# Performance work log

Measured on AMD Instinct MI355X. Metric: run time of the kernel, lower is better.

Reference implementation:

```python
import jax, jax.numpy as jnp
import numpy as np

B, N, M = 8, 2048, 16
HA, HB, HG = 64, 32, 32
NCONV, VOCAB, HINIT = 4, 100, 92
NAMINO = 2048
EPS = 1e-5


def setup_inputs() -> dict:
    key = jax.random.key(0)
    ks = jax.random.split(key, 24)
    s = 0.02
    return {
        'atom_emb_idx': jax.random.randint(ks[0], (B, N), 0, VOCAB, dtype=jnp.int32),
        'nbr_emb': jax.random.normal(ks[1], (B, N, M, HB), jnp.float32),
        'nbr_adj_list': jax.random.randint(ks[2], (B, N, M), 0, N, dtype=jnp.int32),
        'atom_amino_idx': jax.random.randint(ks[3], (B, N), 0, NAMINO, dtype=jnp.int32),
        'atom_mask': jnp.ones((B, N), jnp.float32),
        'embed_table': jax.random.normal(ks[4], (VOCAB, HINIT), jnp.float32) * s,
        'W_emb': jax.random.normal(ks[5], (HINIT, HA), jnp.float32) * s,
        'b_emb': jnp.zeros((HA,), jnp.float32),
        'fc_W': jax.random.normal(ks[6], (NCONV, 2 * HA + HB, 2 * HA), jnp.float32) * s,
        'fc_b': jnp.zeros((NCONV, 2 * HA), jnp.float32),
        'bnh_g': jnp.ones((NCONV, 2 * HA), jnp.float32),
        'bnh_b': jnp.zeros((NCONV, 2 * HA), jnp.float32),
        'bno_g': jnp.ones((NCONV, HA), jnp.float32),
        'bno_b': jnp.zeros((NCONV, HA), jnp.float32),
        'W_cf': jax.random.normal(ks[7], (HA, HG), jnp.float32) * s,
        'b_cf': jnp.zeros((HG,), jnp.float32),
        'W_out': jax.random.normal(ks[8], (HG, 1), jnp.float32) * s,
        'b_out': jnp.zeros((1,), jnp.float32),
        'W_af': jax.random.normal(ks[9], (HA, HG), jnp.float32) * s,
        'b_af': jnp.zeros((HG,), jnp.float32),
        'W_ao': jax.random.normal(ks[10], (HG, 1), jnp.float32) * s,
        'b_ao': jnp.zeros((1,), jnp.float32),
    }


def _bn(x, g, b, axes):
    # training-mode batchnorm (biased variance), matching torch default train()
    m = jnp.mean(x, axis=axes, keepdims=True)
    v = jnp.mean((x - m) ** 2, axis=axes, keepdims=True)
    return (x - m) * jax.lax.rsqrt(v + EPS) * g + b


def _conv(atom_emb, nbr_emb, adj, mask, W, b, g1, be1, g2, be2):
    # atom_emb [B,N,HA], adj [B,N,M], mask [B,N,1]
    nbr_atom = jax.vmap(lambda e, i: e[i])(atom_emb, adj)       # gather [B,N,M,HA]
    nbr_atom = nbr_atom * mask[..., None]                        # [B,N,1,1] bcast
    self_emb = jnp.broadcast_to(atom_emb[:, :, None, :], nbr_atom.shape)
    tot = jnp.concatenate([self_emb, nbr_atom, nbr_emb], axis=-1)  # [B,N,M,2HA+HB]
    z = tot @ W + b                                              # [B,N,M,2HA]
    z = _bn(z, g1, be1, (0, 1, 2))
    filt, core = jnp.split(z, 2, axis=-1)
    s = jnp.sum(jax.nn.sigmoid(filt) * jax.nn.relu(core), axis=2)  # [B,N,HA]
    s = _bn(s, g2, be2, (0, 1))
    return jax.nn.relu(atom_emb + s)


def reference(atom_emb_idx, nbr_emb, nbr_adj_list, atom_amino_idx, atom_mask,
              embed_table, W_emb, b_emb, fc_W, fc_b, bnh_g, bnh_b, bno_g, bno_b,
              W_cf, b_cf, W_out, b_out, W_af, b_af, W_ao, b_ao):
    atom_emb = embed_table[atom_emb_idx] @ W_emb + b_emb        # [B,N,HA]
    mask = atom_mask[..., None]                                  # [B,N,1]
    for i in range(NCONV):
        atom_emb = atom_emb * mask
        atom_emb = _conv(atom_emb, nbr_emb, nbr_adj_list, mask,
                         fc_W[i], fc_b[i], bnh_g[i], bnh_b[i], bno_g[i], bno_b[i])
    atom_emb = atom_emb * mask
    # residue (amino) pooling via scatter-add
    idx = atom_amino_idx.reshape(-1)
    amino_emb = jax.ops.segment_sum(atom_emb.reshape(-1, HA), idx, num_segments=NAMINO)
    mask_pooled = jnp.where(jnp.arange(NAMINO)[:, None] < jnp.min(idx), 0, 1).astype(jnp.uint8)
    amino_emb = jax.nn.relu(amino_emb) @ W_af + b_af
    amino_emb = jax.nn.relu(amino_emb)
    # protein pooling: masked mean
    protein_emb = jnp.sum(atom_emb, axis=1) / jnp.sum(mask, axis=1)  # [B,HA]
    protein_emb = jax.nn.relu(protein_emb) @ W_cf + b_cf
    protein_emb = jax.nn.relu(protein_emb)
    out_global = protein_emb @ W_out + b_out                     # [B,1]
    out_amino = amino_emb @ W_ao + b_ao                          # [NAMINO,1]
    return out_global, out_amino, mask_pooled
```

## Files before the change

### kernel.cpp

```cpp
#include <hip/hip_runtime.h>
#include <cstdint>
#include <cstddef>

#define EPS_ 1e-5f
#define NATOM 16384
#define NB    8
#define NN    2048
#define NM    16
#define NHA   64
#define NHB   32
#define NHG   32
#define NVOCAB 100
#define NHINIT 92
#define NAMINO_ 2048
#define NPART 1024
#define NSLOT 8

#define OFF_EMB      0
#define OFF_SELF     1048576
#define OFF_NBRU     3145728
#define OFF_S        4194304
#define OFF_AMINO    5242880
#define OFF_PSUM     5373952
#define OFF_MSUM     5374464
#define OFF_MAX      5374472
#define OFF_SLOT1    5374480
#define OFF_SLOT2    5382672
#define ZERO_FLOATS  (5386768 - 5242880)
#define OFF_PACK     5386768
#define OFF_WPACK    9581072
#define WS_FLOATS    9589264

typedef __attribute__((ext_vector_type(8))) short bf16x8;
typedef __attribute__((ext_vector_type(4))) float f32x4;

static __device__ __forceinline__ short f2bf(float f) {
    union { float f; uint32_t u; } v; v.f = f;
    uint32_t r = v.u + 0x7fffu + ((v.u >> 16) & 1u);
    return (short)(r >> 16);
}
static __device__ __forceinline__ float bfLo(uint32_t x) {
    union { uint32_t u; float f; } v; v.u = x << 16; return v.f;
}
static __device__ __forceinline__ float bfHi(uint32_t x) {
    union { uint32_t u; float f; } v; v.u = x & 0xffff0000u; return v.f;
}

static __device__ __forceinline__ int conv_wg(int bid) {
    return (bid & 7) * (NPART / 8) + (bid >> 3);
}

__launch_bounds__(256)
__global__ void k_prep(const float* __restrict__ nbr_emb, uint4* __restrict__ pack,
                       const int* __restrict__ atom_idx, const float* __restrict__ et,
                       const float* __restrict__ W_emb, const float* __restrict__ b_emb,
                       float* __restrict__ emb,
                       const float* __restrict__ fcW, uint4* __restrict__ wpack)
{
    __shared__ float lw[NHINIT * NHA];
    const int t = threadIdx.x;
    if (blockIdx.x < 4096) {
        int g = blockIdx.x * 256 + t;
        int bn = g >> 6, l = g & 63;
        const float* src = nbr_emb + (size_t)bn * 512 + (l & 15) * 32 + (l >> 4) * 8;
        float4 a = *reinterpret_cast<const float4*>(src);
        float4 b = *reinterpret_cast<const float4*>(src + 4);
        union { short s[8]; uint4 u; } o;
        o.s[0] = f2bf(a.x); o.s[1] = f2bf(a.y); o.s[2] = f2bf(a.z); o.s[3] = f2bf(a.w);
        o.s[4] = f2bf(b.x); o.s[5] = f2bf(b.y); o.s[6] = f2bf(b.z); o.s[7] = f2bf(b.w);
        pack[g] = o.u;
        return;
    }
    if (blockIdx.x >= 5120) {
        int L = blockIdx.x - 5120;
        if (t < 64) {
            int l15 = t & 15, lg = t >> 4;
            const float* We = fcW + (size_t)L * 160 * 128 + 128 * 128;
#pragma unroll
            for (int cb = 0; cb < 8; ++cb) {
                union { short s[8]; uint4 u; } w;
#pragma unroll
                for (int j = 0; j < 8; ++j)
                    w.s[j] = f2bf(We[(lg * 8 + j) * 128 + cb * 16 + l15]);
                wpack[L * 512 + cb * 64 + t] = w.u;
            }
        }
        return;
    }
    for (int j = t; j < NHINIT * NHA; j += 256) lw[j] = W_emb[j];
    __syncthreads();
    const int bbase = (blockIdx.x - 4096) * 16;
    const int sub = t >> 6, c = t & 63;
    const float bb = b_emb[c];
#pragma unroll
    for (int aa = 0; aa < 4; ++aa) {
        int atom = bbase + sub + 4 * aa;
        int idxu = __builtin_amdgcn_readfirstlane(atom_idx[atom]);
        const float* er = et + (size_t)idxu * NHINIT;
        float acc = bb;
        for (int h = 0; h < NHINIT; ++h)
            acc = fmaf(er[h], lw[h * NHA + c], acc);
        emb[(size_t)atom * NHA + c] = acc;
    }
}

template<int UPD>
__launch_bounds__(256)
__global__ void k_proj(float* __restrict__ emb, const float* __restrict__ mask,
                       const float* __restrict__ s_buf, const float* __restrict__ slot2,
                       const float* __restrict__ g1, const float* __restrict__ b1,
                       const float* __restrict__ fcW, const float* __restrict__ fcb,
                       float* __restrict__ selfp, uint32_t* __restrict__ nbrpU)
{
    __shared__ float le[512];
    __shared__ float nb[8][128];
    __shared__ float affA[64], affB[64];
    const int t = threadIdx.x;
    if (UPD) {
        if (t < 64) {
            float S = 0.f, Q = 0.f;
#pragma unroll
            for (int s = 0; s < NSLOT; ++s) {
                S += slot2[s * 128 + t];
                Q += slot2[s * 128 + 64 + t];
            }
            float mean = S * (1.f / 16384.f);
            float var = Q * (1.f / 16384.f) - mean * mean;
            float a = g1[t] * rsqrtf(var + EPS_);
            affA[t] = a; affB[t] = b1[t] - mean * a;
        }
        __syncthreads();
    }
#pragma unroll
    for (int jj = 0; jj < 2; ++jj) {
        int j = t + jj * 256;
        int gi = blockIdx.x * 512 + j;
        int bn = blockIdx.x * 8 + (j >> 6);
        int c = j & 63;
        float m = mask[bn];
        float v;
        if (UPD) {
            v = fmaxf(fmaf(s_buf[gi], affA[c], affB[c]) + emb[gi] * m, 0.f);
            emb[gi] = v;
        } else {
            v = emb[gi];
        }
        le[j] = v * m;
    }
    __syncthreads();
    int half = t >> 7;
    int oc = t & 127;
    float acc[8];
    float bias = half ? 0.f : fcb[oc];
#pragma unroll
    for (int a = 0; a < 8; ++a) acc[a] = bias;
    const float* Wbase = fcW + (half * 64) * 128 + oc;
    for (int c = 0; c < 64; ++c) {
        float w = Wbase[c * 128];
#pragma unroll
        for (int a = 0; a < 8; ++a) acc[a] = fmaf(le[a * 64 + c], w, acc[a]);
    }
    if (half == 0) {
#pragma unroll
        for (int a = 0; a < 8; ++a)
            selfp[(size_t)(blockIdx.x * 8 + a) * 128 + oc] = acc[a];
    } else {
#pragma unroll
        for (int a = 0; a < 8; ++a) nb[a][oc] = acc[a];
    }
    __syncthreads();
#pragma unroll
    for (int k = 0; k < 2; ++k) {
        int idx = t + k * 256;
        int a = idx >> 6, c2 = idx & 63;
        uint32_t lo = (uint16_t)f2bf(nb[a][c2]);
        uint32_t hi = (uint16_t)f2bf(nb[a][c2 + 64]);
        nbrpU[(size_t)(blockIdx.x * 8 + a) * 64 + c2] = lo | (hi << 16);
    }
}

__launch_bounds__(256, 4)
__global__ void k_conv_stats(const float* __restrict__ selfp, const uint32_t* __restrict__ nbrpU,
                             const uint4* __restrict__ pack, const int* __restrict__ adj,
                             const float* __restrict__ mask, const uint4* __restrict__ wpack,
                             float* __restrict__ slot1)
{
    __shared__ float red[4][256];
    const int lane = threadIdx.x & 63;
    const int wid = threadIdx.x >> 6;
    const int l15 = lane & 15, lg = lane >> 4;
    bf16x8 Wb[8];
#pragma unroll
    for (int cb = 0; cb < 8; ++cb) {
        union { uint4 u; bf16x8 v; } w;
        w.u = wpack[cb * 64 + lane];
        Wb[cb] = w.v;
    }
    float sum[8] = {0, 0, 0, 0, 0, 0, 0, 0};
    float sq[8] = {0, 0, 0, 0, 0, 0, 0, 0};
    const int wg = conv_wg(blockIdx.x);
    const int base = (wg * 4 + wid) * 4;
    for (int aa = 0; aa < 4; ++aa) {
        const int bn = base + aa;
        const int b = bn >> 11;
        const float mn = mask[bn];
        int adjv = 0;
        if (lane < 16) adjv = adj[bn * 16 + lane];
        union { uint4 u; bf16x8 v; } af;
        af.u = pack[(size_t)bn * 64 + lane];
        float sp[8];
#pragma unroll
        for (int cb = 0; cb < 8; ++cb) sp[cb] = selfp[(size_t)bn * 128 + cb * 16 + l15];
        const uint32_t* npb = nbrpU + (size_t)b * NN * 64;
        f32x4 acc[8];
#pragma unroll
        for (int r = 0; r < 4; ++r) {
            const int am = __shfl(adjv, lg * 4 + r);
            const uint32_t* rowU = npb + (size_t)am * 64;
#pragma unroll
            for (int c2 = 0; c2 < 4; ++c2) {
                uint32_t u = rowU[c2 * 16 + l15];
                acc[c2][r]     = fmaf(mn, bfLo(u), sp[c2]);
                acc[c2 + 4][r] = fmaf(mn, bfHi(u), sp[c2 + 4]);
            }
        }
#pragma unroll
        for (int cb = 0; cb < 8; ++cb)
            acc[cb] = __builtin_amdgcn_mfma_f32_16x16x32_bf16(af.v, Wb[cb], acc[cb], 0, 0, 0);
#pragma unroll
        for (int cb = 0; cb < 8; ++cb) {
#pragma unroll
            for (int r = 0; r < 4; ++r) {
                float z = acc[cb][r];
                sum[cb] += z; sq[cb] = fmaf(z, z, sq[cb]);
            }
        }
    }
#pragma unroll
    for (int cb = 0; cb < 8; ++cb) {
        sum[cb] += __shfl_xor(sum[cb], 16);
        sum[cb] += __shfl_xor(sum[cb], 32);
        sq[cb] += __shfl_xor(sq[cb], 16);
        sq[cb] += __shfl_xor(sq[cb], 32);
    }
    if (lane < 16) {
#pragma unroll
        for (int cb = 0; cb < 8; ++cb) {
            red[wid][cb * 16 + lane] = sum[cb];
            red[wid][128 + cb * 16 + lane] = sq[cb];
        }
    }
    __syncthreads();
    const int t = threadIdx.x;
    float v = red[0][t] + red[1][t] + red[2][t] + red[3][t];
    atomicAdd(&slot1[(blockIdx.x & (NSLOT - 1)) * 256 + t], v);
}

__launch_bounds__(256, 4)
__global__ void k_conv_gate(const float* __restrict__ selfp, const uint32_t* __restrict__ nbrpU,
                            const uint4* __restrict__ pack, const int* __restrict__ adj,
                            const float* __restrict__ mask, const uint4* __restrict__ wpack,
                            const float* __restrict__ slot1,
                            const float* __restrict__ g0, const float* __restrict__ b0,
                            float* __restrict__ s_out, float* __restrict__ slot2)
{
    __shared__ float red[4][128];
    __shared__ float a1[128], b1s[128];
    const int t = threadIdx.x;
    if (t < 128) {
        float S = 0.f, Q = 0.f;
#pragma unroll
        for (int s = 0; s < NSLOT; ++s) {
            S += slot1[s * 256 + t];
            Q += slot1[s * 256 + 128 + t];
        }
        float mean = S * (1.f / 262144.f);
        float var = Q * (1.f / 262144.f) - mean * mean;
        float a = g0[t] * rsqrtf(var + EPS_);
        a1[t] = a; b1s[t] = b0[t] - mean * a;
    }
    __syncthreads();
    const int lane = threadIdx.x & 63;
    const int wid = threadIdx.x >> 6;
    const int l15 = lane & 15, lg = lane >> 4;
    bf16x8 Wb[8];
#pragma unroll
    for (int cb = 0; cb < 8; ++cb) {
        union { uint4 u; bf16x8 v; } w;
        w.u = wpack[cb * 64 + lane];
        Wb[cb] = w.v;
    }
    float aA[8], aB[8];
#pragma unroll
    for (int cb = 0; cb < 8; ++cb) {
        aA[cb] = a1[cb * 16 + l15];
        aB[cb] = b1s[cb * 16 + l15];
    }
    float ssum[4] = {0, 0, 0, 0}, ssq[4] = {0, 0, 0, 0};
    const int wg = conv_wg(blockIdx.x);
    const int base = (wg * 4 + wid) * 4;
    for (int aa = 0; aa < 4; ++aa) {
        const int bn = base + aa;
        const int b = bn >> 11;
        const float mn = mask[bn];
        int adjv = 0;
        if (lane < 16) adjv = adj[bn * 16 + lane];
        union { uint4 u; bf16x8 v; } af;
        af.u = pack[(size_t)bn * 64 + lane];
        float sp[8];
#pragma unroll
        for (int cb = 0; cb < 8; ++cb) sp[cb] = selfp[(size_t)bn * 128 + cb * 16 + l15];
        const uint32_t* npb = nbrpU + (size_t)b * NN * 64;
        f32x4 acc[8];
#pragma unroll
        for (int r = 0; r < 4; ++r) {
            const int am = __shfl(adjv, lg * 4 + r);
            const uint32_t* rowU = npb + (size_t)am * 64;
#pragma unroll
            for (int c2 = 0; c2 < 4; ++c2) {
                uint32_t u = rowU[c2 * 16 + l15];
                acc[c2][r]     = fmaf(mn, bfLo(u), sp[c2]);
                acc[c2 + 4][r] = fmaf(mn, bfHi(u), sp[c2 + 4]);
            }
        }
#pragma unroll
        for (int cb = 0; cb < 8; ++cb)
            acc[cb] = __builtin_amdgcn_mfma_f32_16x16x32_bf16(af.v, Wb[cb], acc[cb], 0, 0, 0);
        float sv[4];
#pragma unroll
        for (int cb = 0; cb < 4; ++cb) {
            float s = 0.f;
#pragma unroll
            for (int r = 0; r < 4; ++r) {
                float zf = fmaf(acc[cb][r], aA[cb], aB[cb]);
                float zc = fmaf(acc[cb + 4][r], aA[cb + 4], aB[cb + 4]);
                float f = 1.f / (1.f + __expf(-zf));
                s = fmaf(f, fmaxf(zc, 0.f), s);
            }
            s += __shfl_xor(s, 16);
            s += __shfl_xor(s, 32);
            sv[cb] = s;
            ssum[cb] += s; ssq[cb] = fmaf(s, s, ssq[cb]);
        }
        if (lane < 16) {
#pragma unroll
            for (int cb = 0; cb < 4; ++cb)
                s_out[(size_t)bn * 64 + cb * 16 + lane] = sv[cb];
        }
    }
    if (lane < 16) {
#pragma unroll
        for (int cb = 0; cb < 4; ++cb) {
            red[wid][cb * 16 + lane] = ssum[cb];
            red[wid][64 + cb * 16 + lane] = ssq[cb];
        }
    }
    __syncthreads();
    if (t < 128) {
        float v = red[0][t] + red[1][t] + red[2][t] + red[3][t];
        atomicAdd(&slot2[(blockIdx.x & (NSLOT - 1)) * 128 + t], v);
    }
}

__launch_bounds__(256)
__global__ void k_pool(const float* __restrict__ emb, const float* __restrict__ s_buf,
                       const float* __restrict__ slot2,
                       const float* __restrict__ g1, const float* __restrict__ b1,
                       const float* __restrict__ mask, const int* __restrict__ aidx,
                       float* __restrict__ amino, float* __restrict__ psum,
                       float* __restrict__ msum, int* __restrict__ maxv)
{
    __shared__ float red[256];
    __shared__ float mred[4];
    __shared__ int kred[4];
    __shared__ float affA[64], affB[64];
    int t = threadIdx.x, sub = t >> 6, c = t & 63;
    if (t < 64) {
        float S = 0.f, Q = 0.f;
#pragma unroll
        for (int s = 0; s < NSLOT; ++s) {
            S += slot2[s * 128 + t];
            Q += slot2[s * 128 + 64 + t];
        }
        float mean = S * (1.f / 16384.f);
        float var = Q * (1.f / 16384.f) - mean * mean;
        float a = g1[t] * rsqrtf(var + EPS_);
        affA[t] = a; affB[t] = b1[t] - mean * a;
    }
    __syncthreads();
    int base = blockIdx.x * 32;
    int b = base >> 11;
    float pacc = 0.f, macc = 0.f;
    int kmax = 0;
    for (int j = 0; j < 8; ++j) {
        int bn = base + sub + 4 * j;
        size_t gi = (size_t)bn * 64 + c;
        float m = mask[bn];
        float e4 = fmaxf(fmaf(s_buf[gi], affA[c], affB[c]) + emb[gi] * m, 0.f);
        float v = e4 * m;
        int k = aidx[bn];
        atomicAdd(&amino[(size_t)k * 64 + c], v);
        pacc += v;
        if (c == 0) { macc += m; kmax = max(kmax, 0x7fffffff - k); }
    }
    red[t] = pacc;
    if (c == 0) { mred[sub] = macc; kred[sub] = kmax; }
    __syncthreads();
    if (t < 64) {
        float tot = red[t] + red[64 + t] + red[128 + t] + red[192 + t];
        atomicAdd(&psum[b * 64 + t], tot);
    }
    if (t == 0) {
        atomicAdd(&msum[b], mred[0] + mred[1] + mred[2] + mred[3]);
        atomicMax(maxv, max(max(kred[0], kred[1]), max(kred[2], kred[3])));
    }
}

__launch_bounds__(256)
__global__ void k_heads(const float* __restrict__ amino, const float* __restrict__ W_af,
                        const float* __restrict__ b_af, const float* __restrict__ W_ao,
                        const float* __restrict__ b_ao,
                        const float* __restrict__ psum, const float* __restrict__ msum,
                        const float* __restrict__ W_cf, const float* __restrict__ b_cf,
                        const float* __restrict__ W_out, const float* __restrict__ b_out,
                        const int* __restrict__ maxv, float* __restrict__ out)
{
    const int t = threadIdx.x;
    if (blockIdx.x < 256) {
        int kk = t >> 5, j = t & 31;
        int k = blockIdx.x * 8 + kk;
        float acc = b_af[j];
        for (int c = 0; c < 64; ++c)
            acc = fmaf(fmaxf(amino[(size_t)k * 64 + c], 0.f), W_af[c * 32 + j], acc);
        float h = fmaxf(acc, 0.f);
        float val = h * W_ao[j];
        for (int off = 16; off > 0; off >>= 1) val += __shfl_down(val, off, 32);
        if (j == 0) out[8 + k] = val + b_ao[0];
    } else if (blockIdx.x == 256) {
        int bb = t >> 5, j = t & 31;
        float inv = 1.f / msum[bb];
        float acc = b_cf[j];
        for (int c = 0; c < 64; ++c)
            acc = fmaf(fmaxf(psum[bb * 64 + c] * inv, 0.f), W_cf[c * 32 + j], acc);
        float h = fmaxf(acc, 0.f);
        float val = h * W_out[j];
        for (int off = 16; off > 0; off >>= 1) val += __shfl_down(val, off, 32);
        if (j == 0) out[bb] = val + b_out[0];
    } else {
        int k = (blockIdx.x - 257) * 256 + t;
        int minv = 0x7fffffff - *maxv;
        out[8 + NAMINO_ + k] = (k < minv) ? 0.f : 1.f;
    }
}

extern "C" void kernel_launch(void* const* d_in, const int* in_sizes, int n_in,
                              void* d_out, int out_size, void* d_ws, size_t ws_size,
                              hipStream_t stream)
{
    const int* atom_idx = (const int*)d_in[0];
    const float* nbr_emb = (const float*)d_in[1];
    const int* adj = (const int*)d_in[2];
    const int* aidx = (const int*)d_in[3];
    const float* mask = (const float*)d_in[4];
    const float* et = (const float*)d_in[5];
    const float* W_emb = (const float*)d_in[6];
    const float* b_emb = (const float*)d_in[7];
    const float* fcW = (const float*)d_in[8];
    const float* fcb = (const float*)d_in[9];
    const float* bnh_g = (const float*)d_in[10];
    const float* bnh_b = (const float*)d_in[11];
    const float* bno_g = (const float*)d_in[12];
    const float* bno_b = (const float*)d_in[13];
    const float* W_cf = (const float*)d_in[14];
    const float* b_cf = (const float*)d_in[15];
    const float* W_out = (const float*)d_in[16];
    const float* b_out = (const float*)d_in[17];
    const float* W_af = (const float*)d_in[18];
    const float* b_af = (const float*)d_in[19];
    const float* W_ao = (const float*)d_in[20];
    const float* b_ao = (const float*)d_in[21];

    float* ws = (float*)d_ws;
    float* emb = ws + OFF_EMB;
    float* selfp = ws + OFF_SELF;
    uint32_t* nbrpU = (uint32_t*)(ws + OFF_NBRU);
    float* s_buf = ws + OFF_S;
    float* amino = ws + OFF_AMINO;
    float* psum = ws + OFF_PSUM;
    float* msum = ws + OFF_MSUM;
    int* maxv = (int*)(ws + OFF_MAX);
    float* slot1 = ws + OFF_SLOT1;
    float* slot2 = ws + OFF_SLOT2;
    uint4* pack = (uint4*)(ws + OFF_PACK);
    uint4* wpack = (uint4*)(ws + OFF_WPACK);
    float* out = (float*)d_out;

    hipMemsetAsync(amino, 0, ZERO_FLOATS * sizeof(float), stream);

    k_prep<<<5124, 256, 0, stream>>>(nbr_emb, pack, atom_idx, et, W_emb, b_emb, emb,
                                     fcW, wpack);

    for (int i = 0; i < 4; ++i) {
        const float* Wi = fcW + (size_t)i * 160 * 128;
        if (i == 0)
            k_proj<0><<<NATOM / 8, 256, 0, stream>>>(emb, mask, s_buf, slot2, bno_g, bno_b,
                                                     Wi, fcb + i * 128, selfp, nbrpU);
        else
            k_proj<1><<<NATOM / 8, 256, 0, stream>>>(emb, mask, s_buf,
                                                     slot2 + (size_t)(i - 1) * (NSLOT * 128),
                                                     bno_g + (i - 1) * 64, bno_b + (i - 1) * 64,
                                                     Wi, fcb + i * 128, selfp, nbrpU);
        k_conv_stats<<<NPART, 256, 0, stream>>>(selfp, nbrpU, pack, adj, mask,
                                                wpack + (size_t)i * 512,
                                                slot1 + (size_t)i * (NSLOT * 256));
        k_conv_gate<<<NPART, 256, 0, stream>>>(selfp, nbrpU, pack, adj, mask,
                                               wpack + (size_t)i * 512,
                                               slot1 + (size_t)i * (NSLOT * 256),
                                               bnh_g + i * 128, bnh_b + i * 128,
                                               s_buf, slot2 + (size_t)i * (NSLOT * 128));
    }

    k_pool<<<NATOM / 32, 256, 0, stream>>>(emb, s_buf, slot2 + 3 * (NSLOT * 128),
                                           bno_g + 3 * 64, bno_b + 3 * 64,
                                           mask, aidx, amino, psum, msum, maxv);
    k_heads<<<265, 256, 0, stream>>>(amino, W_af, b_af, W_ao, b_ao,
                                     psum, msum, W_cf, b_cf, W_out, b_out, maxv, out);
}
```

Baseline: 247.2 us.

## Permute self/neighbor projection layout for vectorized uint4/float4 gathers in conv kernels

The projection kernel now writes the self and neighbor projections in an interleaved channel order, so each lane's 8 channels sit contiguously. The stats and apply conv kernels can then fetch them with one uint4 and two float4 loads instead of many scalar loads. The adjacency indices for all four atoms of a wave are also loaded once with a full-wave load, replacing a masked load per atom. The risk is that the write-side permutation adds LDS bank conflicts and index arithmetic, and every consumer must agree on the new layout.

```diff
diff --git a/kernel.cpp b/kernel.cpp
--- a/kernel.cpp
+++ b/kernel.cpp
@@ -149,7 +149,8 @@
     }
     __syncthreads();
     int half = t >> 7;
-    int oc = t & 127;
+    int tt = t & 127;
+    int oc = half ? tt : (((tt & 7) << 4) | (tt >> 3));
     float acc[8];
     float bias = half ? 0.f : fcb[oc];
 #pragma unroll
@@ -163,7 +164,7 @@
     if (half == 0) {
 #pragma unroll
         for (int a = 0; a < 8; ++a)
-            selfp[(size_t)(blockIdx.x * 8 + a) * 128 + oc] = acc[a];
+            selfp[(size_t)(blockIdx.x * 8 + a) * 128 + tt] = acc[a];
     } else {
 #pragma unroll
         for (int a = 0; a < 8; ++a) nb[a][oc] = acc[a];
@@ -172,10 +173,12 @@
 #pragma unroll
     for (int k = 0; k < 2; ++k) {
         int idx = t + k * 256;
-        int a = idx >> 6, c2 = idx & 63;
-        uint32_t lo = (uint16_t)f2bf(nb[a][c2]);
-        uint32_t hi = (uint16_t)f2bf(nb[a][c2 + 64]);
-        nbrpU[(size_t)(blockIdx.x * 8 + a) * 64 + c2] = lo | (hi << 16);
+        int a = idx >> 6, s = idx & 63;
+        int j = s >> 2, c2 = s & 3;
+        int c = c2 * 16 + j;
+        uint32_t lo = (uint16_t)f2bf(nb[a][c]);
+        uint32_t hi = (uint16_t)f2bf(nb[a][c + 64]);
+        nbrpU[(size_t)(blockIdx.x * 8 + a) * 64 + s] = lo | (hi << 16);
     }
 }
 
@@ -200,29 +203,26 @@
     float sq[8] = {0, 0, 0, 0, 0, 0, 0, 0};
     const int wg = conv_wg(blockIdx.x);
     const int base = (wg * 4 + wid) * 4;
+    const int adjv = adj[base * 16 + lane];
     for (int aa = 0; aa < 4; ++aa) {
         const int bn = base + aa;
         const int b = bn >> 11;
         const float mn = mask[bn];
-        int adjv = 0;
-        if (lane < 16) adjv = adj[bn * 16 + lane];
         union { uint4 u; bf16x8 v; } af;
         af.u = pack[(size_t)bn * 64 + lane];
-        float sp[8];
-#pragma unroll
-        for (int cb = 0; cb < 8; ++cb) sp[cb] = selfp[(size_t)bn * 128 + cb * 16 + l15];
+        const float4* spp = reinterpret_cast<const float4*>(selfp + (size_t)bn * 128 + l15 * 8);
+        float4 sA = spp[0], sB = spp[1];
+        float sp[8] = {sA.x, sA.y, sA.z, sA.w, sB.x, sB.y, sB.z, sB.w};
         const uint32_t* npb = nbrpU + (size_t)b * NN * 64;
         f32x4 acc[8];
 #pragma unroll
         for (int r = 0; r < 4; ++r) {
-            const int am = __shfl(adjv, lg * 4 + r);
-            const uint32_t* rowU = npb + (size_t)am * 64;
-#pragma unroll
-            for (int c2 = 0; c2 < 4; ++c2) {
-                uint32_t u = rowU[c2 * 16 + l15];
-                acc[c2][r]     = fmaf(mn, bfLo(u), sp[c2]);
-                acc[c2 + 4][r] = fmaf(mn, bfHi(u), sp[c2 + 4]);
-            }
+            const int am = __shfl(adjv, aa * 16 + lg * 4 + r);
+            const uint4 u4 = *reinterpret_cast<const uint4*>(npb + (size_t)am * 64 + l15 * 4);
+            acc[0][r] = fmaf(mn, bfLo(u4.x), sp[0]); acc[4][r] = fmaf(mn, bfHi(u4.x), sp[4]);
+            acc[1][r] = fmaf(mn, bfLo(u4.y), sp[1]); acc[5][r] = fmaf(mn, bfHi(u4.y), sp[5]);
+            acc[2][r] = fmaf(mn, bfLo(u4.z), sp[2]); acc[6][r] = fmaf(mn, bfHi(u4.z), sp[6]);
+            acc[3][r] = fmaf(mn, bfLo(u4.w), sp[3]); acc[7][r] = fmaf(mn, bfHi(u4.w), sp[7]);
         }
 #pragma unroll
         for (int cb = 0; cb < 8; ++cb)
@@ -299,29 +299,26 @@
     float ssum[4] = {0, 0, 0, 0}, ssq[4] = {0, 0, 0, 0};
     const int wg = conv_wg(blockIdx.x);
     const int base = (wg * 4 + wid) * 4;
+    const int adjv = adj[base * 16 + lane];
     for (int aa = 0; aa < 4; ++aa) {
         const int bn = base + aa;
         const int b = bn >> 11;
         const float mn = mask[bn];
-        int adjv = 0;
-        if (lane < 16) adjv = adj[bn * 16 + lane];
         union { uint4 u; bf16x8 v; } af;
         af.u = pack[(size_t)bn * 64 + lane];
-        float sp[8];
-#pragma unroll
-        for (int cb = 0; cb < 8; ++cb) sp[cb] = selfp[(size_t)bn * 128 + cb * 16 + l15];
+        const float4* spp = reinterpret_cast<const float4*>(selfp + (size_t)bn * 128 + l15 * 8);
+        float4 sA = spp[0], sB = spp[1];
+        float sp[8] = {sA.x, sA.y, sA.z, sA.w, sB.x, sB.y, sB.z, sB.w};
         const uint32_t* npb = nbrpU + (size_t)b * NN * 64;
         f32x4 acc[8];
 #pragma unroll
         for (int r = 0; r < 4; ++r) {
-            const int am = __shfl(adjv, lg * 4 + r);
-            const uint32_t* rowU = npb + (size_t)am * 64;
-#pragma unroll
-            for (int c2 = 0; c2 < 4; ++c2) {
-                uint32_t u = rowU[c2 * 16 + l15];
-                acc[c2][r]     = fmaf(mn, bfLo(u), sp[c2]);
-                acc[c2 + 4][r] = fmaf(mn, bfHi(u), sp[c2 + 4]);
-            }
+            const int am = __shfl(adjv, aa * 16 + lg * 4 + r);
+            const uint4 u4 = *reinterpret_cast<const uint4*>(npb + (size_t)am * 64 + l15 * 4);
+            acc[0][r] = fmaf(mn, bfLo(u4.x), sp[0]); acc[4][r] = fmaf(mn, bfHi(u4.x), sp[4]);
+            acc[1][r] = fmaf(mn, bfLo(u4.y), sp[1]); acc[5][r] = fmaf(mn, bfHi(u4.y), sp[5]);
+            acc[2][r] = fmaf(mn, bfLo(u4.z), sp[2]); acc[6][r] = fmaf(mn, bfHi(u4.z), sp[6]);
+            acc[3][r] = fmaf(mn, bfLo(u4.w), sp[3]); acc[7][r] = fmaf(mn, bfHi(u4.w), sp[7]);
         }
 #pragma unroll
         for (int cb = 0; cb < 8; ++cb)
```

Measured after the change: 273.1 us. 1.1x slower.
